# Performance work log

Hardware: AMD Instinct MI355X
Metric: run time of the kernel (lower is better)

The kernel has to match this reference:

```python
import jax, jax.numpy as jnp
import numpy as np

N, H, T, HID = 2, 8, 1024, 64
EMBED_DIM = H * HID  # 512, out_proj dim
EPS = 1e-6


def setup_inputs() -> dict:
    key = jax.random.key(0)
    kq, kk, kv, kw, kb = jax.random.split(key, 5)
    q = jax.random.normal(kq, (N, H, T, HID), jnp.float32)
    k = jax.random.normal(kk, (N, H, T, HID), jnp.float32)
    v = jax.random.normal(kv, (N, H, T, HID), jnp.float32)
    W_out = jax.random.normal(kw, (EMBED_DIM, EMBED_DIM), jnp.float32) / np.float32(np.sqrt(EMBED_DIM))
    b_out = jax.random.normal(kb, (EMBED_DIM,), jnp.float32) * 0.02
    return {"q": q, "k": k, "v": v, "W_out": W_out, "b_out": b_out}


def reference(q, k, v, W_out, b_out):
    # cosFormer attention, causal=True, act_fun='relu', has_outproj=True
    n, h, t, hid = q.shape
    nh = n * h
    m = t  # max(src_len, tgt_len)

    # q/k: permute(2,0,1,3).view(T,N,H*HID) -> relu -> view(-1,N*H,HID).transpose(0,1)
    # is equivalent to a direct reshape (N,H,T,HID)->(N*H,T,HID) since relu is elementwise.
    qr = jax.nn.relu(q).reshape(nh, t, hid)
    kr = jax.nn.relu(k).reshape(nh, t, hid)
    # v: original does v.view(-1, N*H, HID).transpose(0,1) WITHOUT permuting first
    # (reinterprets the (N,H,T,HID) buffer as (T, N*H, HID)); reproduce faithfully.
    vr = jnp.swapaxes(v.reshape(t, nh, hid), 0, 1)  # (NH, T, HID)

    # cos/sin position reweighting: weight_index = pi/2 * arange(1..m), used as /m
    idx = (np.float32(np.pi / 2) * jnp.arange(1, t + 1, dtype=q.dtype)) / m  # (T,)
    s = jnp.sin(idx)[None, :, None]
    c = jnp.cos(idx)[None, :, None]
    q_ = jnp.concatenate([qr * s, qr * c], axis=-1)  # (NH, T, 2*HID)
    k_ = jnp.concatenate([kr * s, kr * c], axis=-1)  # (NH, T, 2*HID)

    # causal path: cumulative outer products k_ (x) v, then contract with q_
    kv = jnp.einsum('nld,nlm->nldm', k_, vr)          # (NH, T, 2*HID, HID)
    kv_cum = jnp.cumsum(kv, axis=1)
    qkv = jnp.einsum('nld,nldm->nlm', q_, kv_cum)     # (NH, T, HID)
    k_cum = jnp.cumsum(k_, axis=1)
    denom = jnp.maximum(jnp.einsum('nld,nld->nl', q_, k_cum), EPS)
    attn = qkv / denom[..., None]                     # (NH, T, HID)

    # (NH,T,HID) -> (T,N,H*HID), out_proj, back to (N,H,T,HID)
    attn = jnp.swapaxes(attn, 0, 1).reshape(t, n, h * hid)
    attn = attn @ W_out.T + b_out
    context = attn.reshape(t, n, h, hid).transpose(1, 2, 0, 3)  # (N,H,T,HID)
    probs = jnp.zeros((n, h, t, t), q.dtype)
    return context, probs
```

## Files before the change

### kernel.cpp

```cpp
#include <hip/hip_runtime.h>

#define TSEQ 1024
#define HIDV 64
#define NHEADS 16
#define LCH 64
#define NCH 16
#define EMBED 512
#define CTX_FLOATS (NHEADS * TSEQ * HIDV)
#define EPSV 1e-6f
#define PIH 1.5707963267948966f

typedef short bf16x8 __attribute__((ext_vector_type(8)));
typedef float f32x4 __attribute__((ext_vector_type(4)));

__device__ __forceinline__ float relu_f(float x) { return fmaxf(x, 0.0f); }
__device__ __forceinline__ ushort f2bf(float f) {
    uint u = __float_as_uint(f);
    u += 0x7FFF + ((u >> 16) & 1);
    return (ushort)(u >> 16);
}
__device__ __forceinline__ float bf2f(ushort h) { return __uint_as_float(((uint)h) << 16); }
__device__ __forceinline__ uint pk2(float a, float b) {
    return (uint)f2bf(a) | ((uint)f2bf(b) << 16);
}

__global__ __launch_bounds__(256) void k1_chunksum(
    const float* __restrict__ K, const float* __restrict__ V,
    ushort* __restrict__ S16, float* __restrict__ ksumws,
    float4* __restrict__ probs4)
{
    __shared__ ushort kwT[128 * 88];
    __shared__ ushort vT1[32 * 88];
    const int bid = blockIdx.x;
    const int tid = threadIdx.x;

    {
        float4 z = make_float4(0.f, 0.f, 0.f, 0.f);
        size_t base = (size_t)bid * 2048 + tid;
        #pragma unroll
        for (int s = 0; s < 8; ++s) probs4[base + s * 256] = z;
    }

    const int pair = bid >> 1, mh = bid & 1, m0b = mh * 32;
    const int b = pair >> 4, c = pair & 15;
    const int l0 = c * LCH;

    #pragma unroll
    for (int s = 0; s < 4; ++s) {
        int e = tid + s * 256;
        int i = e >> 4, d = (e & 15) * 4;
        float4 k4 = *(const float4*)(K + (size_t)(b * TSEQ + l0 + i) * HIDV + d);
        float si, ci;
        __sincosf(PIH * (float)(l0 + i + 1) * (1.0f / 1024.0f), &si, &ci);
        float kv[4] = {relu_f(k4.x), relu_f(k4.y), relu_f(k4.z), relu_f(k4.w)};
        #pragma unroll
        for (int j = 0; j < 4; ++j) {
            kwT[(d + j) * 88 + i] = f2bf(si * kv[j]);
            kwT[(d + 64 + j) * 88 + i] = f2bf(ci * kv[j]);
        }
    }
    #pragma unroll
    for (int s = 0; s < 2; ++s) {
        int e = tid + s * 256;
        int i = e >> 3, mf = (e & 7) * 4;
        float4 v4 = *(const float4*)(V + ((size_t)(l0 + i) * NHEADS + b) * HIDV + m0b + mf);
        vT1[(mf + 0) * 88 + i] = f2bf(v4.x);
        vT1[(mf + 1) * 88 + i] = f2bf(v4.y);
        vT1[(mf + 2) * 88 + i] = f2bf(v4.z);
        vT1[(mf + 3) * 88 + i] = f2bf(v4.w);
    }
    __syncthreads();

    const int w = tid >> 6, lane = tid & 63;
    const int quad = lane >> 4, l15 = lane & 15;

    bf16x8 bfv[2][2];
    #pragma unroll
    for (int mt = 0; mt < 2; ++mt)
        #pragma unroll
        for (int kk = 0; kk < 2; ++kk)
            bfv[mt][kk] = *(const bf16x8*)(vT1 + (mt * 16 + l15) * 88 + kk * 32 + quad * 8);

    f32x4 acc[2][2];
    #pragma unroll
    for (int ii = 0; ii < 2; ++ii)
        #pragma unroll
        for (int mt = 0; mt < 2; ++mt) acc[ii][mt] = (f32x4){0.f, 0.f, 0.f, 0.f};
    #pragma unroll
    for (int ii = 0; ii < 2; ++ii) {
        int itv = w + ii * 4;
        #pragma unroll
        for (int kk = 0; kk < 2; ++kk) {
            bf16x8 af = *(const bf16x8*)(kwT + (itv * 16 + l15) * 88 + kk * 32 + quad * 8);
            #pragma unroll
            for (int mt = 0; mt < 2; ++mt)
                acc[ii][mt] = __builtin_amdgcn_mfma_f32_16x16x32_bf16(af, bfv[mt][kk], acc[ii][mt], 0, 0, 0);
        }
    }
    ushort* SpT = S16 + (size_t)pair * 8192;
    #pragma unroll
    for (int ii = 0; ii < 2; ++ii)
        #pragma unroll
        for (int mt = 0; mt < 2; ++mt) {
            int m = m0b + mt * 16 + l15;
            int ddb = (w + ii * 4) * 16 + quad * 4;
            uint2 pk = make_uint2(pk2(acc[ii][mt][0], acc[ii][mt][1]),
                                  pk2(acc[ii][mt][2], acc[ii][mt][3]));
            *(uint2*)(SpT + m * 128 + ddb) = pk;
        }
    if (mh == 0 && tid < 128) {
        float ssum = 0.f;
        #pragma unroll
        for (int ss = 0; ss < 8; ++ss) {
            uint4 u = *(const uint4*)(kwT + tid * 88 + ss * 8);
            ssum += bf2f((ushort)(u.x & 0xffff)) + bf2f((ushort)(u.x >> 16));
            ssum += bf2f((ushort)(u.y & 0xffff)) + bf2f((ushort)(u.y >> 16));
            ssum += bf2f((ushort)(u.z & 0xffff)) + bf2f((ushort)(u.z >> 16));
            ssum += bf2f((ushort)(u.w & 0xffff)) + bf2f((ushort)(u.w >> 16));
        }
        ksumws[(size_t)pair * 128 + tid] = ssum;
    }
}

__global__ __launch_bounds__(256) void k2_scan(
    const ushort* __restrict__ S16, float* __restrict__ ksumws,
    ushort* __restrict__ Ptg, const float* __restrict__ W,
    ushort* __restrict__ W16, float4* __restrict__ probs4)
{
    {
        float4 z = make_float4(0.f, 0.f, 0.f, 0.f);
        size_t base = 1048576 + (size_t)blockIdx.x * 2048 + threadIdx.x;
        #pragma unroll
        for (int s = 0; s < 8; ++s) probs4[base + s * 256] = z;
    }
    int g = blockIdx.x * 256 + threadIdx.x;
    {
        int bs = g >> 13, idx = g & 8191;
        const ushort* Sp = S16 + (size_t)bs * 131072 + idx;
        ushort* Pp = Ptg + (size_t)bs * 131072 + idx;
        float acc = 0.f;
        #pragma unroll
        for (int c = 0; c < NCH; ++c) {
            float t = bf2f(Sp[c * 8192]);
            Pp[c * 8192] = f2bf(acc);
            acc += t;
        }
    }
    if (g < 65536) {
        float4 w4 = *(const float4*)(W + (size_t)g * 4);
        *(uint2*)(W16 + (size_t)g * 4) = make_uint2(pk2(w4.x, w4.y), pk2(w4.z, w4.w));
    }
    if (g < NHEADS * 128) {
        int b2 = g >> 7, i2 = g & 127;
        float a2 = 0.f;
        #pragma unroll
        for (int c = 0; c < NCH; ++c) {
            float* p = ksumws + (size_t)(b2 * NCH + c) * 128 + i2;
            float t = *p; *p = a2; a2 += t;
        }
    }
}

#define SMEM_BYTES 58368
#define OFF_QW 0
#define OFF_KW 17408
#define OFF_PT 34816
#define OFF_VT 43520
#define OFF_AM 48128
#define OFF_PSUM 57344
#define OFF_DENA 57856
#define OFF_DENI 58112

__global__ __launch_bounds__(256) void k3_attn(
    const float* __restrict__ Q, const float* __restrict__ K,
    const float* __restrict__ V,
    const ushort* __restrict__ Ptg, const float* __restrict__ ksumws,
    ushort* __restrict__ attn216, float4* __restrict__ probs4)
{
    __shared__ __align__(16) char smem[SMEM_BYTES];
    ushort* qw = (ushort*)(smem + OFF_QW);
    ushort* kw = (ushort*)(smem + OFF_KW);
    ushort* Pt = (ushort*)(smem + OFF_PT);
    ushort* vT = (ushort*)(smem + OFF_VT);
    ushort* Am = (ushort*)(smem + OFF_AM);
    float* psum = (float*)(smem + OFF_PSUM);
    float* denA = (float*)(smem + OFF_DENA);
    float* denI = (float*)(smem + OFF_DENI);

    const int bid = blockIdx.x;
    const int tid = threadIdx.x;
    const int w = tid >> 6, lane = tid & 63;
    const int quad = lane >> 4, l15 = lane & 15;

    {
        float4 z = make_float4(0.f, 0.f, 0.f, 0.f);
        size_t base = 2097152 + (size_t)bid * 2048 + tid;
        #pragma unroll
        for (int s = 0; s < 8; ++s) probs4[base + s * 256] = z;
    }

    const int pair = bid >> 1, mh = bid & 1, m0b = mh * 32;
    const int b = pair >> 4, c = pair & 15;
    const int l0 = c * LCH;

    #pragma unroll
    for (int s = 0; s < 4; ++s) {
        int e = tid + s * 256;
        int i = e >> 4, d = (e & 15) * 4;
        float si, ci;
        __sincosf(PIH * (float)(l0 + i + 1) * (1.0f / 1024.0f), &si, &ci);
        float4 q4 = *(const float4*)(Q + (size_t)(b * TSEQ + l0 + i) * HIDV + d);
        float qv[4] = {relu_f(q4.x), relu_f(q4.y), relu_f(q4.z), relu_f(q4.w)};
        *(uint2*)(qw + i * 136 + d) = make_uint2(pk2(si * qv[0], si * qv[1]), pk2(si * qv[2], si * qv[3]));
        *(uint2*)(qw + i * 136 + 64 + d) = make_uint2(pk2(ci * qv[0], ci * qv[1]), pk2(ci * qv[2], ci * qv[3]));
        float4 k4 = *(const float4*)(K + (size_t)(b * TSEQ + l0 + i) * HIDV + d);
        float kv[4] = {relu_f(k4.x), relu_f(k4.y), relu_f(k4.z), relu_f(k4.w)};
        *(uint2*)(kw + i * 136 + d) = make_uint2(pk2(si * kv[0], si * kv[1]), pk2(si * kv[2], si * kv[3]));
        *(uint2*)(kw + i * 136 + 64 + d) = make_uint2(pk2(ci * kv[0], ci * kv[1]), pk2(ci * kv[2], ci * kv[3]));
    }
    {
        const ushort* Pg = Ptg + (size_t)pair * 8192;
        #pragma unroll
        for (int s = 0; s < 2; ++s) {
            int e = tid + s * 256;
            int mrow = e >> 4, dd8 = (e & 15) * 8;
            *(uint4*)(Pt + mrow * 136 + dd8) = *(const uint4*)(Pg + (m0b + mrow) * 128 + dd8);
        }
    }
    #pragma unroll
    for (int s = 0; s < 2; ++s) {
        int e = tid + s * 256;
        int j = e >> 3, mf = (e & 7) * 4;
        float4 v4 = *(const float4*)(V + ((size_t)(l0 + j) * NHEADS + b) * HIDV + m0b + mf);
        vT[(mf + 0) * 72 + j] = f2bf(v4.x);
        vT[(mf + 1) * 72 + j] = f2bf(v4.y);
        vT[(mf + 2) * 72 + j] = f2bf(v4.z);
        vT[(mf + 3) * 72 + j] = f2bf(v4.w);
    }
    if (tid < 128) psum[tid] = ksumws[(size_t)pair * 128 + tid];
    __syncthreads();

    const int it = w;
    bf16x8 af[4];
    #pragma unroll
    for (int kk = 0; kk < 4; ++kk)
        af[kk] = *(const bf16x8*)(qw + (it * 16 + l15) * 136 + kk * 32 + quad * 8);

    f32x4 accA[4];
    #pragma unroll
    for (int jt = 0; jt < 4; ++jt) {
        accA[jt] = (f32x4){0.f, 0.f, 0.f, 0.f};
        #pragma unroll
        for (int kk = 0; kk < 4; ++kk) {
            bf16x8 bf = *(const bf16x8*)(kw + (jt * 16 + l15) * 136 + kk * 32 + quad * 8);
            accA[jt] = __builtin_amdgcn_mfma_f32_16x16x32_bf16(af[kk], bf, accA[jt], 0, 0, 0);
        }
    }
    {
        float rsum[4] = {0.f, 0.f, 0.f, 0.f};
        #pragma unroll
        for (int jt = 0; jt < 4; ++jt) {
            int j = jt * 16 + l15;
            #pragma unroll
            for (int r = 0; r < 4; ++r) {
                int i = it * 16 + quad * 4 + r;
                float val = (j <= i) ? accA[jt][r] : 0.f;
                Am[i * 72 + j] = f2bf(val);
                rsum[r] += val;
            }
        }
        #pragma unroll
        for (int off = 1; off < 16; off <<= 1) {
            rsum[0] += __shfl_xor(rsum[0], off);
            rsum[1] += __shfl_xor(rsum[1], off);
            rsum[2] += __shfl_xor(rsum[2], off);
            rsum[3] += __shfl_xor(rsum[3], off);
        }
        if (l15 == 0) {
            #pragma unroll
            for (int r = 0; r < 4; ++r) denA[it * 16 + quad * 4 + r] = rsum[r];
        }
    }
    if (tid < 64) {
        float s = 0.f;
        #pragma unroll
        for (int ss = 0; ss < 16; ++ss) {
            uint4 u = *(const uint4*)(qw + tid * 136 + ss * 8);
            s += bf2f((ushort)(u.x & 0xffff)) * psum[ss * 8 + 0] + bf2f((ushort)(u.x >> 16)) * psum[ss * 8 + 1];
            s += bf2f((ushort)(u.y & 0xffff)) * psum[ss * 8 + 2] + bf2f((ushort)(u.y >> 16)) * psum[ss * 8 + 3];
            s += bf2f((ushort)(u.z & 0xffff)) * psum[ss * 8 + 4] + bf2f((ushort)(u.z >> 16)) * psum[ss * 8 + 5];
            s += bf2f((ushort)(u.w & 0xffff)) * psum[ss * 8 + 6] + bf2f((ushort)(u.w >> 16)) * psum[ss * 8 + 7];
        }
        denI[tid] = s;
    }
    __syncthreads();

    f32x4 accO[2];
    #pragma unroll
    for (int mm = 0; mm < 2; ++mm) {
        accO[mm] = (f32x4){0.f, 0.f, 0.f, 0.f};
        #pragma unroll
        for (int kk = 0; kk < 4; ++kk) {
            bf16x8 bp = *(const bf16x8*)(Pt + (mm * 16 + l15) * 136 + kk * 32 + quad * 8);
            accO[mm] = __builtin_amdgcn_mfma_f32_16x16x32_bf16(af[kk], bp, accO[mm], 0, 0, 0);
        }
    }
    bf16x8 aA[2];
    #pragma unroll
    for (int kk = 0; kk < 2; ++kk)
        aA[kk] = *(const bf16x8*)(Am + (it * 16 + l15) * 72 + kk * 32 + quad * 8);
    #pragma unroll
    for (int mm = 0; mm < 2; ++mm)
        #pragma unroll
        for (int kk = 0; kk < 2; ++kk) {
            bf16x8 bv = *(const bf16x8*)(vT + (mm * 16 + l15) * 72 + kk * 32 + quad * 8);
            accO[mm] = __builtin_amdgcn_mfma_f32_16x16x32_bf16(aA[kk], bv, accO[mm], 0, 0, 0);
        }

    const int nb = b >> 3, hh = b & 7;
    #pragma unroll
    for (int r = 0; r < 4; ++r) {
        int i = it * 16 + quad * 4 + r;
        float inv = 1.0f / fmaxf(denA[i] + denI[i], EPSV);
        #pragma unroll
        for (int mm = 0; mm < 2; ++mm) {
            int m = m0b + mm * 16 + l15;
            attn216[(size_t)((l0 + i) * 2 + nb) * EMBED + hh * 64 + m] = f2bf(accO[mm][r] * inv);
        }
    }
}

__global__ __launch_bounds__(256) void k4_outproj(
    const ushort* __restrict__ A16, const ushort* __restrict__ W16,
    const float* __restrict__ bias, float* __restrict__ out,
    float4* __restrict__ probs4)
{
    __shared__ ushort Ab[32 * 72];
    __shared__ ushort Bb[64 * 72];
    const int bid = blockIdx.x;
    const int tid = threadIdx.x;
    {
        float4 z = make_float4(0.f, 0.f, 0.f, 0.f);
        size_t base = 3145728 + (size_t)bid * 2048 + tid;
        #pragma unroll
        for (int s = 0; s < 8; ++s) probs4[base + s * 256] = z;
    }
    const int rt = bid >> 3, et = bid & 7;
    const int r0 = rt * 32, e0 = et * 64;
    const int w = tid >> 6, lane = tid & 63;
    const int quad = lane >> 4, l15 = lane & 15;
    const int it4 = w >> 1, jt0 = (w & 1) * 2;
    f32x4 acc4[2];
    acc4[0] = (f32x4){0.f, 0.f, 0.f, 0.f};
    acc4[1] = (f32x4){0.f, 0.f, 0.f, 0.f};

    for (int f0 = 0; f0 < EMBED; f0 += 64) {
        __syncthreads();
        {
            int rr = tid >> 3, ff = (tid & 7) * 8;
            *(uint4*)(Ab + rr * 72 + ff) = *(const uint4*)(A16 + (size_t)(r0 + rr) * EMBED + f0 + ff);
        }
        #pragma unroll
        for (int s = 0; s < 2; ++s) {
            int e = tid + s * 256;
            int rr = e >> 3, ff = (e & 7) * 8;
            *(uint4*)(Bb + rr * 72 + ff) = *(const uint4*)(W16 + (size_t)(e0 + rr) * EMBED + f0 + ff);
        }
        __syncthreads();
        bf16x8 af2[2];
        #pragma unroll
        for (int kk = 0; kk < 2; ++kk)
            af2[kk] = *(const bf16x8*)(Ab + (it4 * 16 + l15) * 72 + kk * 32 + quad * 8);
        #pragma unroll
        for (int jj = 0; jj < 2; ++jj) {
            int jt = jt0 + jj;
            #pragma unroll
            for (int kk = 0; kk < 2; ++kk) {
                bf16x8 bf = *(const bf16x8*)(Bb + (jt * 16 + l15) * 72 + kk * 32 + quad * 8);
                acc4[jj] = __builtin_amdgcn_mfma_f32_16x16x32_bf16(af2[kk], bf, acc4[jj], 0, 0, 0);
            }
        }
    }
    #pragma unroll
    for (int jj = 0; jj < 2; ++jj) {
        int e = e0 + (jt0 + jj) * 16 + l15;
        float be = bias[e];
        int h = e >> 6, m = e & 63;
        #pragma unroll
        for (int r = 0; r < 4; ++r) {
            int rr = r0 + it4 * 16 + quad * 4 + r;
            int t = rr >> 1, n = rr & 1;
            out[((size_t)(n * 8 + h) * TSEQ + t) * HIDV + m] = acc4[jj][r] + be;
        }
    }
}

extern "C" void kernel_launch(void* const* d_in, const int* in_sizes, int n_in,
                              void* d_out, int out_size, void* d_ws, size_t ws_size,
                              hipStream_t stream) {
    const float* q = (const float*)d_in[0];
    const float* k = (const float*)d_in[1];
    const float* v = (const float*)d_in[2];
    const float* W = (const float*)d_in[3];
    const float* bias = (const float*)d_in[4];
    float* out = (float*)d_out;
    float* ws = (float*)d_ws;

    ushort* S16 = (ushort*)ws;
    float* ksum_ws = ws + 1048576;
    ushort* Ptg = (ushort*)(ws + 1081344);
    ushort* attn216 = (ushort*)(ws + 2129920);
    ushort* W16 = (ushort*)(ws + 2654208);
    float4* probs4 = (float4*)(out + CTX_FLOATS);

    k1_chunksum<<<dim3(512), dim3(256), 0, stream>>>(k, v, S16, ksum_ws, probs4);
    k2_scan<<<dim3(512), dim3(256), 0, stream>>>(S16, ksum_ws, Ptg, W, W16, probs4);
    k3_attn<<<dim3(512), dim3(256), 0, stream>>>(q, k, v, Ptg, ksum_ws, attn216, probs4);
    k4_outproj<<<dim3(512), dim3(256), 0, stream>>>(attn216, W16, bias, out, probs4);
}
```

Before: 113.5 us.

## Fold chunk prefix scan into attention kernel and drop separate scan launch

Removes the standalone scan kernel: each attention block now sums the preceding chunks' bf16 state and k-sums itself, straight from the per-chunk workspace. The W bf16 conversion moves into the first kernel, and the probs zeroing is spread over three kernels instead of four. This saves one launch and the write and re-read of the prefix buffer. In exchange, later chunks redundantly re-read up to 15 chunk states, adding memory traffic and load imbalance across blocks.

```diff
diff --git a/kernel.cpp b/kernel.cpp
--- a/kernel.cpp
+++ b/kernel.cpp
@@ -24,10 +24,11 @@
     return (uint)f2bf(a) | ((uint)f2bf(b) << 16);
 }
 
-__global__ __launch_bounds__(256) void k1_chunksum(
+__global__ __launch_bounds__(256) void kA_chunksum(
     const float* __restrict__ K, const float* __restrict__ V,
+    const float* __restrict__ W,
     ushort* __restrict__ S16, float* __restrict__ ksumws,
-    float4* __restrict__ probs4)
+    ushort* __restrict__ W16, float4* __restrict__ probs4)
 {
     __shared__ ushort kwT[128 * 88];
     __shared__ ushort vT1[32 * 88];
@@ -36,9 +37,16 @@
 
     {
         float4 z = make_float4(0.f, 0.f, 0.f, 0.f);
-        size_t base = (size_t)bid * 2048 + tid;
-        #pragma unroll
-        for (int s = 0; s < 8; ++s) probs4[base + s * 256] = z;
+        size_t base = (size_t)bid * 2560 + tid;
+        #pragma unroll
+        for (int s = 0; s < 10; ++s) probs4[base + s * 256] = z;
+    }
+    {
+        int g = bid * 128 + (tid & 127);
+        if (tid < 128) {
+            float4 w4 = *(const float4*)(W + (size_t)g * 4);
+            *(uint2*)(W16 + (size_t)g * 4) = make_uint2(pk2(w4.x, w4.y), pk2(w4.z, w4.w));
+        }
     }
 
     const int pair = bid >> 1, mh = bid & 1, m0b = mh * 32;
@@ -119,45 +127,6 @@
             ssum += bf2f((ushort)(u.w & 0xffff)) + bf2f((ushort)(u.w >> 16));
         }
         ksumws[(size_t)pair * 128 + tid] = ssum;
-    }
-}
-
-__global__ __launch_bounds__(256) void k2_scan(
-    const ushort* __restrict__ S16, float* __restrict__ ksumws,
-    ushort* __restrict__ Ptg, const float* __restrict__ W,
-    ushort* __restrict__ W16, float4* __restrict__ probs4)
-{
-    {
-        float4 z = make_float4(0.f, 0.f, 0.f, 0.f);
-        size_t base = 1048576 + (size_t)blockIdx.x * 2048 + threadIdx.x;
-        #pragma unroll
-        for (int s = 0; s < 8; ++s) probs4[base + s * 256] = z;
-    }
-    int g = blockIdx.x * 256 + threadIdx.x;
-    {
-        int bs = g >> 13, idx = g & 8191;
-        const ushort* Sp = S16 + (size_t)bs * 131072 + idx;
-        ushort* Pp = Ptg + (size_t)bs * 131072 + idx;
-        float acc = 0.f;
-        #pragma unroll
-        for (int c = 0; c < NCH; ++c) {
-            float t = bf2f(Sp[c * 8192]);
-            Pp[c * 8192] = f2bf(acc);
-            acc += t;
-        }
-    }
-    if (g < 65536) {
-        float4 w4 = *(const float4*)(W + (size_t)g * 4);
-        *(uint2*)(W16 + (size_t)g * 4) = make_uint2(pk2(w4.x, w4.y), pk2(w4.z, w4.w));
-    }
-    if (g < NHEADS * 128) {
-        int b2 = g >> 7, i2 = g & 127;
-        float a2 = 0.f;
-        #pragma unroll
-        for (int c = 0; c < NCH; ++c) {
-            float* p = ksumws + (size_t)(b2 * NCH + c) * 128 + i2;
-            float t = *p; *p = a2; a2 += t;
-        }
     }
 }
 
@@ -171,10 +140,10 @@
 #define OFF_DENA 57856
 #define OFF_DENI 58112
 
-__global__ __launch_bounds__(256) void k3_attn(
+__global__ __launch_bounds__(256) void kB_attn(
     const float* __restrict__ Q, const float* __restrict__ K,
     const float* __restrict__ V,
-    const ushort* __restrict__ Ptg, const float* __restrict__ ksumws,
+    const ushort* __restrict__ S16, const float* __restrict__ ksumws,
     ushort* __restrict__ attn216, float4* __restrict__ probs4)
 {
     __shared__ __align__(16) char smem[SMEM_BYTES];
@@ -194,14 +163,44 @@
 
     {
         float4 z = make_float4(0.f, 0.f, 0.f, 0.f);
-        size_t base = 2097152 + (size_t)bid * 2048 + tid;
-        #pragma unroll
-        for (int s = 0; s < 8; ++s) probs4[base + s * 256] = z;
+        size_t base = 1310720 + (size_t)bid * 2560 + tid;
+        #pragma unroll
+        for (int s = 0; s < 10; ++s) probs4[base + s * 256] = z;
     }
 
     const int pair = bid >> 1, mh = bid & 1, m0b = mh * 32;
     const int b = pair >> 4, c = pair & 15;
     const int l0 = c * LCH;
+
+    {
+        const int ml = tid >> 3, dd0 = (tid & 7) * 16;
+        const ushort* Sb = S16 + ((size_t)b * NCH) * 8192 + (m0b + ml) * 128 + dd0;
+        float accp[16];
+        #pragma unroll
+        for (int u = 0; u < 16; ++u) accp[u] = 0.f;
+        for (int cp = 0; cp < c; ++cp) {
+            const ushort* Sp = Sb + (size_t)cp * 8192;
+            uint4 u0 = *(const uint4*)(Sp);
+            uint4 u1 = *(const uint4*)(Sp + 8);
+            uint uu[8] = {u0.x, u0.y, u0.z, u0.w, u1.x, u1.y, u1.z, u1.w};
+            #pragma unroll
+            for (int p = 0; p < 8; ++p) {
+                accp[p * 2 + 0] += bf2f((ushort)(uu[p] & 0xffff));
+                accp[p * 2 + 1] += bf2f((ushort)(uu[p] >> 16));
+            }
+        }
+        uint pkv[8];
+        #pragma unroll
+        for (int p = 0; p < 8; ++p) pkv[p] = pk2(accp[p * 2], accp[p * 2 + 1]);
+        *(uint4*)(Pt + ml * 136 + dd0) = make_uint4(pkv[0], pkv[1], pkv[2], pkv[3]);
+        *(uint4*)(Pt + ml * 136 + dd0 + 8) = make_uint4(pkv[4], pkv[5], pkv[6], pkv[7]);
+    }
+    if (tid < 128) {
+        float s = 0.f;
+        const float* Kb = ksumws + (size_t)b * NCH * 128 + tid;
+        for (int cp = 0; cp < c; ++cp) s += Kb[cp * 128];
+        psum[tid] = s;
+    }
 
     #pragma unroll
     for (int s = 0; s < 4; ++s) {
@@ -218,15 +217,6 @@
         *(uint2*)(kw + i * 136 + d) = make_uint2(pk2(si * kv[0], si * kv[1]), pk2(si * kv[2], si * kv[3]));
         *(uint2*)(kw + i * 136 + 64 + d) = make_uint2(pk2(ci * kv[0], ci * kv[1]), pk2(ci * kv[2], ci * kv[3]));
     }
-    {
-        const ushort* Pg = Ptg + (size_t)pair * 8192;
-        #pragma unroll
-        for (int s = 0; s < 2; ++s) {
-            int e = tid + s * 256;
-            int mrow = e >> 4, dd8 = (e & 15) * 8;
-            *(uint4*)(Pt + mrow * 136 + dd8) = *(const uint4*)(Pg + (m0b + mrow) * 128 + dd8);
-        }
-    }
     #pragma unroll
     for (int s = 0; s < 2; ++s) {
         int e = tid + s * 256;
@@ -237,7 +227,6 @@
         vT[(mf + 2) * 72 + j] = f2bf(v4.z);
         vT[(mf + 3) * 72 + j] = f2bf(v4.w);
     }
-    if (tid < 128) psum[tid] = ksumws[(size_t)pair * 128 + tid];
     __syncthreads();
 
     const int it = w;
@@ -330,7 +319,7 @@
     }
 }
 
-__global__ __launch_bounds__(256) void k4_outproj(
+__global__ __launch_bounds__(256) void kC_outproj(
     const ushort* __restrict__ A16, const ushort* __restrict__ W16,
     const float* __restrict__ bias, float* __restrict__ out,
     float4* __restrict__ probs4)
@@ -341,9 +330,9 @@
     const int tid = threadIdx.x;
     {
         float4 z = make_float4(0.f, 0.f, 0.f, 0.f);
-        size_t base = 3145728 + (size_t)bid * 2048 + tid;
-        #pragma unroll
-        for (int s = 0; s < 8; ++s) probs4[base + s * 256] = z;
+        size_t base = 2621440 + (size_t)bid * 3072 + tid;
+        #pragma unroll
+        for (int s = 0; s < 12; ++s) probs4[base + s * 256] = z;
     }
     const int rt = bid >> 3, et = bid & 7;
     const int r0 = rt * 32, e0 = et * 64;
@@ -408,13 +397,11 @@
 
     ushort* S16 = (ushort*)ws;
     float* ksum_ws = ws + 1048576;
-    ushort* Ptg = (ushort*)(ws + 1081344);
-    ushort* attn216 = (ushort*)(ws + 2129920);
-    ushort* W16 = (ushort*)(ws + 2654208);
+    ushort* attn216 = (ushort*)(ws + 1081344);
+    ushort* W16 = (ushort*)(ws + 1605632);
     float4* probs4 = (float4*)(out + CTX_FLOATS);
 
-    k1_chunksum<<<dim3(512), dim3(256), 0, stream>>>(k, v, S16, ksum_ws, probs4);
-    k2_scan<<<dim3(512), dim3(256), 0, stream>>>(S16, ksum_ws, Ptg, W, W16, probs4);
-    k3_attn<<<dim3(512), dim3(256), 0, stream>>>(q, k, v, Ptg, ksum_ws, attn216, probs4);
-    k4_outproj<<<dim3(512), dim3(256), 0, stream>>>(attn216, W16, bias, out, probs4);
-}
+    kA_chunksum<<<dim3(512), dim3(256), 0, stream>>>(k, v, W, S16, ksum_ws, W16, probs4);
+    kB_attn<<<dim3(512), dim3(256), 0, stream>>>(q, k, v, S16, ksum_ws, attn216, probs4);
+    kC_outproj<<<dim3(512), dim3(256), 0, stream>>>(attn216, W16, bias, out, probs4);
+}
```

Measured after the change: 113.1 us. About the same (-0.4%).
